# Optimization experiments

Measured on AMD Instinct MI355X. Metric: run time of the kernel, lower is better.

The kernel has to match this reference:

```python
import jax, jax.numpy as jnp
import numpy as np

MARGIN = 1.0
EPS = 1e-6  # torch F.pairwise_distance default eps
B, C, D = 16384, 1000, 1024


def setup_inputs() -> dict:
    key = jax.random.key(0)
    k1, k2, k3 = jax.random.split(key, 3)
    inputs = jax.random.normal(k1, (B, D), dtype=jnp.float32)
    labels = jax.random.randint(k2, (B,), 0, C, dtype=jnp.int64)
    target = jax.random.normal(k3, (C, D), dtype=jnp.float32)
    return {"inputs": inputs, "labels": labels, "target": target}


def _pairdist(a, b):
    # torch F.pairwise_distance(p=2): ||a - b + eps||_2 along last dim
    d = a - b + EPS
    return jnp.sqrt(jnp.sum(d * d, axis=-1))


def reference(inputs, labels, target):
    # --- negative mining: full [B, C] distance matrix via GEMM identity ---
    # (eps is a uniform per-component shift; it does not change the argmin in practice,
    #  and mining indices are non-differentiable anyway)
    x2 = jnp.sum(inputs * inputs, axis=-1, keepdims=True)          # [B, 1]
    t2 = jnp.sum(target * target, axis=-1)                          # [C]
    d2 = x2 - 2.0 * (inputs @ target.T) + t2[None, :]               # [B, C]
    d2 = jnp.maximum(d2, 0.0)
    # exclude the anchor's own class (tx == anchor_label skipped in torch loop)
    own = jax.nn.one_hot(labels, C, dtype=jnp.bool_)                 # [B, C]
    d2 = jnp.where(own, jnp.inf, d2)
    neg_idx = jnp.argmin(d2, axis=-1)                                # [B]

    positive = target[labels]                                        # [B, D]
    negative = target[neg_idx]                                       # [B, D]

    d_ap = _pairdist(inputs, positive)                               # [B]
    d_an = _pairdist(inputs, negative)                               # [B]
    per_anchor = jnp.maximum(d_ap - d_an + MARGIN, 0.0)
    # every anchor forms a valid triplet (C > 1), so total/valid == mean
    return jnp.mean(per_anchor)
```

## Files before the change

kernel.cpp:

```cpp
#include <hip/hip_runtime.h>
#include <hip/hip_bf16.h>

#define NB 16384
#define NC 1000
#define NCP 1024
#define ND 1024
#define BM 64
#define BN 256
#define KSTEPS 32
#define NCB 4

typedef __attribute__((ext_vector_type(8))) short bf16x8;
typedef __attribute__((ext_vector_type(4))) float f32x4;

typedef __attribute__((address_space(1))) const void GV;
typedef __attribute__((address_space(3))) void LV;

__device__ __forceinline__ unsigned short f2bf(float f) {
  union { float f; unsigned u; } c; c.f = f;
  unsigned b = c.u;
  return (unsigned short)((b + 0x7fffu + ((b >> 16) & 1u)) >> 16);
}
__device__ __forceinline__ unsigned pk2(float lo, float hi) {
  return ((unsigned)f2bf(hi) << 16) | (unsigned)f2bf(lo);
}

__global__ __launch_bounds__(256) void prep_kernel(const float* __restrict__ Tf,
                                                   unsigned short* __restrict__ Tb,
                                                   float* __restrict__ t2) {
  const int c = blockIdx.x;
  const int tid = threadIdx.x;
  if (c >= NC) {
    ushort4 z; z.x = z.y = z.z = z.w = 0;
    ((ushort4*)(Tb + (size_t)c * ND))[tid] = z;
    if (tid == 0) t2[c] = 1e30f;
    return;
  }
  float4 v = ((const float4*)(Tf + (size_t)c * ND))[tid];
  float ss = v.x * v.x + v.y * v.y + v.z * v.z + v.w * v.w;
  ushort4 o;
  o.x = f2bf(v.x); o.y = f2bf(v.y); o.z = f2bf(v.z); o.w = f2bf(v.w);
  ((ushort4*)(Tb + (size_t)c * ND))[tid] = o;
  #pragma unroll
  for (int m = 1; m < 64; m <<= 1) ss += __shfl_xor(ss, m, 64);
  __shared__ float red[4];
  if ((tid & 63) == 0) red[tid >> 6] = ss;
  __syncthreads();
  if (tid == 0) t2[c] = red[0] + red[1] + red[2] + red[3];
}

__global__ __launch_bounds__(256, 3) void mine3_kernel(
    const float* __restrict__ X, const int* __restrict__ labels,
    const unsigned short* __restrict__ Tb, const float* __restrict__ t2g,
    float* __restrict__ x2g, float* __restrict__ slab, float2* __restrict__ pairs) {
  __shared__ char sA[2][BM * 64];
  __shared__ char sB[2][BN * 64];
  __shared__ int sLab[BM];
  __shared__ float2 sMin[BM][4];

  const int tid = threadIdx.x;
  const int lane = tid & 63;
  const int wc = tid >> 6;
  const int l15 = lane & 15, l4 = lane >> 4;

  const int bid = (int)blockIdx.x;
  const int wgid = (bid & 7) * 128 + (bid >> 3);
  const int rb = wgid >> 2, cb = wgid & 3;
  const int rowbase = rb * BM, colbase = cb * BN;

  if (tid < BM) sLab[tid] = labels[rowbase + tid];

  const float* aptr = X + (size_t)(rowbase + (tid >> 2)) * ND + ((tid & 3) << 3);
  float ss = 0.0f;
  float4 rA0, rA1;

  auto loadA = [&](int kt) {
    rA0 = *(const float4*)(aptr + kt * 32);
    rA1 = *(const float4*)(aptr + kt * 32 + 4);
  };
  auto writeA = [&](int buf) {
    if (cb == 0) {
      ss += rA0.x * rA0.x + rA0.y * rA0.y + rA0.z * rA0.z + rA0.w * rA0.w
          + rA1.x * rA1.x + rA1.y * rA1.y + rA1.z * rA1.z + rA1.w * rA1.w;
    }
    uint4 w;
    w.x = pk2(rA0.x, rA0.y); w.y = pk2(rA0.z, rA0.w);
    w.z = pk2(rA1.x, rA1.y); w.w = pk2(rA1.z, rA1.w);
    *(uint4*)(sA[buf] + tid * 16) = w;
  };
  auto stageB = [&](int buf, int kt) {
    #pragma unroll
    for (int i = 0; i < 4; ++i) {
      const int o = i * 4096 + tid * 16;
      const char* src = (const char*)Tb + (size_t)(colbase + (o >> 6)) * 2048 + kt * 64 + (o & 63);
      __builtin_amdgcn_global_load_lds((GV*)src, (LV*)(sB[buf] + o), 16, 0, 0);
    }
  };

  f32x4 acc[4][4] = {};

  loadA(0);
  stageB(0, 0);
  writeA(0);
  loadA(1);
  __builtin_amdgcn_sched_barrier(0);
  asm volatile("s_waitcnt vmcnt(2) lgkmcnt(0)\n\ts_barrier" ::: "memory");
  __builtin_amdgcn_sched_barrier(0);

  int cur = 0;
  for (int ks = 0; ks < KSTEPS; ++ks) {
    if (ks + 1 < KSTEPS) {
      writeA(cur ^ 1);
      stageB(cur ^ 1, ks + 1);
      const int kn = (ks + 2 < KSTEPS) ? ks + 2 : KSTEPS - 1;
      loadA(kn);
    }
    const char* pa = sA[cur];
    const char* pb = sB[cur];
    bf16x8 af[4];
    #pragma unroll
    for (int m = 0; m < 4; ++m)
      af[m] = *(const bf16x8*)(pa + ((m * 16 + l15) * 64 + l4 * 16));
    #pragma unroll
    for (int n = 0; n < 4; ++n) {
      bf16x8 bfr = *(const bf16x8*)(pb + ((wc * 64 + n * 16 + l15) * 64 + l4 * 16));
      #pragma unroll
      for (int m = 0; m < 4; ++m)
        acc[m][n] = __builtin_amdgcn_mfma_f32_16x16x32_bf16(af[m], bfr, acc[m][n], 0, 0, 0);
    }
    __builtin_amdgcn_sched_barrier(0);
    asm volatile("s_waitcnt vmcnt(2) lgkmcnt(0)\n\ts_barrier" ::: "memory");
    __builtin_amdgcn_sched_barrier(0);
    cur ^= 1;
  }

  if (cb == 0) {
    ss += __shfl_xor(ss, 1, 64);
    ss += __shfl_xor(ss, 2, 64);
    if ((tid & 3) == 0) x2g[rowbase + (tid >> 2)] = ss;
  }

  float t2v[4];
  #pragma unroll
  for (int n = 0; n < 4; ++n) t2v[n] = t2g[colbase + wc * 64 + n * 16 + l15];

  #pragma unroll
  for (int m = 0; m < 4; ++m) {
    #pragma unroll
    for (int j = 0; j < 4; ++j) {
      const int rowl = m * 16 + l4 * 4 + j;
      const int lab = sLab[rowl];
      float bv = 3.0e38f; int bi = 0x7fffffff;
      #pragma unroll
      for (int n = 0; n < 4; ++n) {
        const int col = colbase + wc * 64 + n * 16 + l15;
        const float sc = t2v[n] - 2.0f * acc[m][n][j];
        if (col == lab) slab[rowbase + rowl] = sc;
        const float sce = (col == lab) ? 3.2e38f : sc;
        if (sce < bv || (sce == bv && col < bi)) { bv = sce; bi = col; }
      }
      #pragma unroll
      for (int mk = 1; mk < 16; mk <<= 1) {
        const float ov = __shfl_xor(bv, mk, 64);
        const int   oi = __shfl_xor(bi, mk, 64);
        if (ov < bv || (ov == bv && oi < bi)) { bv = ov; bi = oi; }
      }
      if (l15 == 0) sMin[rowl][wc] = make_float2(bv, __int_as_float(bi));
    }
  }
  __syncthreads();
  if (tid < BM) {
    float2 p = sMin[tid][0];
    #pragma unroll
    for (int q = 1; q < 4; ++q) {
      float2 o = sMin[tid][q];
      if (o.x < p.x || (o.x == p.x && __float_as_int(o.y) < __float_as_int(p.y))) p = o;
    }
    pairs[(size_t)(rowbase + tid) * NCB + cb] = p;
  }
}

__global__ __launch_bounds__(256) void finalize_kernel(
    const float2* __restrict__ pairs, const float* __restrict__ slab,
    const float* __restrict__ x2g, float* __restrict__ out) {
  const int r = blockIdx.x * 256 + threadIdx.x;
  float2 p = pairs[(size_t)r * NCB];
  #pragma unroll
  for (int q = 1; q < NCB; ++q) {
    float2 o = pairs[(size_t)r * NCB + q];
    if (o.x < p.x || (o.x == p.x && __float_as_int(o.y) < __float_as_int(p.y))) p = o;
  }
  const float x2v = x2g[r];
  const float dap = sqrtf(fmaxf(x2v + slab[r], 0.0f));
  const float dan = sqrtf(fmaxf(x2v + p.x, 0.0f));
  float h = fmaxf(dap - dan + 1.0f, 0.0f);
  #pragma unroll
  for (int mk = 1; mk < 64; mk <<= 1) h += __shfl_xor(h, mk, 64);
  __shared__ float red[4];
  if ((threadIdx.x & 63) == 0) red[threadIdx.x >> 6] = h;
  __syncthreads();
  if (threadIdx.x == 0)
    atomicAdd(out, (red[0] + red[1] + red[2] + red[3]) * (1.0f / (float)NB));
}

extern "C" void kernel_launch(void* const* d_in, const int* in_sizes, int n_in,
                              void* d_out, int out_size, void* d_ws, size_t ws_size,
                              hipStream_t stream) {
  const float* X = (const float*)d_in[0];
  const int* labels = (const int*)d_in[1];
  const float* Tf = (const float*)d_in[2];
  float* out = (float*)d_out;

  char* ws = (char*)d_ws;
  unsigned short* Tb = (unsigned short*)ws;
  float* t2   = (float*)(ws + 2097152);
  float* x2   = (float*)(ws + 2097152 + 4096);
  float* slab = (float*)(ws + 2097152 + 4096 + 65536);
  float2* pairs = (float2*)(ws + 2097152 + 4096 + 131072);

  hipMemsetAsync(d_out, 0, sizeof(float), stream);
  prep_kernel<<<NCP, 256, 0, stream>>>(Tf, Tb, t2);
  mine3_kernel<<<(NB / BM) * NCB, 256, 0, stream>>>(X, labels, Tb, t2, x2, slab, pairs);
  finalize_kernel<<<NB / 256, 256, 0, stream>>>(pairs, slab, x2, out);
}
```

Measured before the change: 180.9 us.

## Reshape mining GEMM tile to 128x128 with a 2x2 wave grid

Changes the workgroup tile from 64 rows by 256 classes to 128 rows by 128 classes. The four waves now form a 2x2 grid instead of splitting only along columns, and the number of column blocks doubles to 8. This halves the per-block B staging, raises the occupancy hint to 4 blocks per CU, and adjusts the vmcnt waits and prefetch ordering to match the larger A load. In exchange, each fp32 input row is now read by twice as many blocks, and the per-row partial minima written out for the finalize pass double.

```diff
diff --git a/kernel.cpp b/kernel.cpp
--- a/kernel.cpp
+++ b/kernel.cpp
@@ -5,10 +5,10 @@
 #define NC 1000
 #define NCP 1024
 #define ND 1024
-#define BM 64
-#define BN 256
+#define BM 128
+#define BN 128
 #define KSTEPS 32
-#define NCB 4
+#define NCB 8
 
 typedef __attribute__((ext_vector_type(8))) short bf16x8;
 typedef __attribute__((ext_vector_type(4))) float f32x4;
@@ -49,50 +49,58 @@
   if (tid == 0) t2[c] = red[0] + red[1] + red[2] + red[3];
 }
 
-__global__ __launch_bounds__(256, 3) void mine3_kernel(
+__global__ __launch_bounds__(256, 4) void fused_kernel(
     const float* __restrict__ X, const int* __restrict__ labels,
     const unsigned short* __restrict__ Tb, const float* __restrict__ t2g,
     float* __restrict__ x2g, float* __restrict__ slab, float2* __restrict__ pairs) {
   __shared__ char sA[2][BM * 64];
   __shared__ char sB[2][BN * 64];
   __shared__ int sLab[BM];
-  __shared__ float2 sMin[BM][4];
+  __shared__ float2 sMin[BM][2];
 
   const int tid = threadIdx.x;
   const int lane = tid & 63;
-  const int wc = tid >> 6;
+  const int wid = tid >> 6;
   const int l15 = lane & 15, l4 = lane >> 4;
+  const int wr = wid >> 1, wc = wid & 1;
 
   const int bid = (int)blockIdx.x;
   const int wgid = (bid & 7) * 128 + (bid >> 3);
-  const int rb = wgid >> 2, cb = wgid & 3;
+  const int rb = wgid >> 3, cb = wgid & 7;
   const int rowbase = rb * BM, colbase = cb * BN;
 
   if (tid < BM) sLab[tid] = labels[rowbase + tid];
 
-  const float* aptr = X + (size_t)(rowbase + (tid >> 2)) * ND + ((tid & 3) << 3);
+  const float* aptr = X + (size_t)(rowbase + (tid >> 1)) * ND + ((tid & 1) << 4);
+  float4 rA[4];
   float ss = 0.0f;
-  float4 rA0, rA1;
 
   auto loadA = [&](int kt) {
-    rA0 = *(const float4*)(aptr + kt * 32);
-    rA1 = *(const float4*)(aptr + kt * 32 + 4);
+    const float4* p = (const float4*)(aptr + kt * 32);
+    rA[0] = p[0]; rA[1] = p[1]; rA[2] = p[2]; rA[3] = p[3];
   };
   auto writeA = [&](int buf) {
     if (cb == 0) {
-      ss += rA0.x * rA0.x + rA0.y * rA0.y + rA0.z * rA0.z + rA0.w * rA0.w
-          + rA1.x * rA1.x + rA1.y * rA1.y + rA1.z * rA1.z + rA1.w * rA1.w;
-    }
-    uint4 w;
-    w.x = pk2(rA0.x, rA0.y); w.y = pk2(rA0.z, rA0.w);
-    w.z = pk2(rA1.x, rA1.y); w.w = pk2(rA1.z, rA1.w);
-    *(uint4*)(sA[buf] + tid * 16) = w;
+      #pragma unroll
+      for (int q = 0; q < 4; ++q)
+        ss += rA[q].x * rA[q].x + rA[q].y * rA[q].y
+            + rA[q].z * rA[q].z + rA[q].w * rA[q].w;
+    }
+    uint4 w0, w1;
+    w0.x = pk2(rA[0].x, rA[0].y); w0.y = pk2(rA[0].z, rA[0].w);
+    w0.z = pk2(rA[1].x, rA[1].y); w0.w = pk2(rA[1].z, rA[1].w);
+    w1.x = pk2(rA[2].x, rA[2].y); w1.y = pk2(rA[2].z, rA[2].w);
+    w1.z = pk2(rA[3].x, rA[3].y); w1.w = pk2(rA[3].z, rA[3].w);
+    char* d = sA[buf] + (tid >> 1) * 64 + ((tid & 1) << 5);
+    *(uint4*)d = w0;
+    *(uint4*)(d + 16) = w1;
   };
   auto stageB = [&](int buf, int kt) {
     #pragma unroll
-    for (int i = 0; i < 4; ++i) {
+    for (int i = 0; i < 2; ++i) {
       const int o = i * 4096 + tid * 16;
-      const char* src = (const char*)Tb + (size_t)(colbase + (o >> 6)) * 2048 + kt * 64 + (o & 63);
+      const char* src = (const char*)Tb + (size_t)(colbase + (o >> 6)) * 2048
+                        + kt * 64 + (o & 63);
       __builtin_amdgcn_global_load_lds((GV*)src, (LV*)(sB[buf] + o), 16, 0, 0);
     }
   };
@@ -104,23 +112,22 @@
   writeA(0);
   loadA(1);
   __builtin_amdgcn_sched_barrier(0);
-  asm volatile("s_waitcnt vmcnt(2) lgkmcnt(0)\n\ts_barrier" ::: "memory");
+  asm volatile("s_waitcnt vmcnt(4) lgkmcnt(0)\n\ts_barrier" ::: "memory");
   __builtin_amdgcn_sched_barrier(0);
 
   int cur = 0;
   for (int ks = 0; ks < KSTEPS; ++ks) {
     if (ks + 1 < KSTEPS) {
+      stageB(cur ^ 1, ks + 1);
       writeA(cur ^ 1);
-      stageB(cur ^ 1, ks + 1);
-      const int kn = (ks + 2 < KSTEPS) ? ks + 2 : KSTEPS - 1;
-      loadA(kn);
+      if (ks + 2 < KSTEPS) loadA(ks + 2);
     }
     const char* pa = sA[cur];
     const char* pb = sB[cur];
     bf16x8 af[4];
     #pragma unroll
     for (int m = 0; m < 4; ++m)
-      af[m] = *(const bf16x8*)(pa + ((m * 16 + l15) * 64 + l4 * 16));
+      af[m] = *(const bf16x8*)(pa + ((wr * 64 + m * 16 + l15) * 64 + l4 * 16));
     #pragma unroll
     for (int n = 0; n < 4; ++n) {
       bf16x8 bfr = *(const bf16x8*)(pb + ((wc * 64 + n * 16 + l15) * 64 + l4 * 16));
@@ -129,15 +136,17 @@
         acc[m][n] = __builtin_amdgcn_mfma_f32_16x16x32_bf16(af[m], bfr, acc[m][n], 0, 0, 0);
     }
     __builtin_amdgcn_sched_barrier(0);
-    asm volatile("s_waitcnt vmcnt(2) lgkmcnt(0)\n\ts_barrier" ::: "memory");
+    if (ks < KSTEPS - 2)
+      asm volatile("s_waitcnt vmcnt(4) lgkmcnt(0)\n\ts_barrier" ::: "memory");
+    else if (ks == KSTEPS - 2)
+      asm volatile("s_waitcnt vmcnt(0) lgkmcnt(0)\n\ts_barrier" ::: "memory");
     __builtin_amdgcn_sched_barrier(0);
     cur ^= 1;
   }
 
   if (cb == 0) {
     ss += __shfl_xor(ss, 1, 64);
-    ss += __shfl_xor(ss, 2, 64);
-    if ((tid & 3) == 0) x2g[rowbase + (tid >> 2)] = ss;
+    if ((tid & 1) == 0) x2g[rowbase + (tid >> 1)] = ss;
   }
 
   float t2v[4];
@@ -148,7 +157,7 @@
   for (int m = 0; m < 4; ++m) {
     #pragma unroll
     for (int j = 0; j < 4; ++j) {
-      const int rowl = m * 16 + l4 * 4 + j;
+      const int rowl = wr * 64 + m * 16 + l4 * 4 + j;
       const int lab = sLab[rowl];
       float bv = 3.0e38f; int bi = 0x7fffffff;
       #pragma unroll
@@ -171,9 +180,8 @@
   __syncthreads();
   if (tid < BM) {
     float2 p = sMin[tid][0];
-    #pragma unroll
-    for (int q = 1; q < 4; ++q) {
-      float2 o = sMin[tid][q];
+    {
+      float2 o = sMin[tid][1];
       if (o.x < p.x || (o.x == p.x && __float_as_int(o.y) < __float_as_int(p.y))) p = o;
     }
     pairs[(size_t)(rowbase + tid) * NCB + cb] = p;
@@ -220,6 +228,6 @@
 
   hipMemsetAsync(d_out, 0, sizeof(float), stream);
   prep_kernel<<<NCP, 256, 0, stream>>>(Tf, Tb, t2);
-  mine3_kernel<<<(NB / BM) * NCB, 256, 0, stream>>>(X, labels, Tb, t2, x2, slab, pairs);
+  fused_kernel<<<(NB / BM) * NCB, 256, 0, stream>>>(X, labels, Tb, t2, x2, slab, pairs);
   finalize_kernel<<<NB / 256, 256, 0, stream>>>(pairs, slab, x2, out);
 }
```

Result: faster. 167.7 us (-7.3%).
